# Optimization experiments

Hardware: AMD Instinct MI355X
Metric: run time of the kernel (lower is better)

## Reference

```python
import jax, jax.numpy as jnp
import numpy as np

B = 16384
QD = 2048   # query_dim
KD = 1024   # key_dim
HID = 1024  # hidden_dim = min(QD, KD)
NH = 16     # num_heads
HD = HID // NH  # head_dim = 64
LN_EPS = 1e-5


def _ln(x, w, b):
    m = jnp.mean(x, axis=-1, keepdims=True)
    v = jnp.mean((x - m) ** 2, axis=-1, keepdims=True)
    return (x - m) * jax.lax.rsqrt(v + LN_EPS) * w + b


def _lin(x, W, b):
    return x @ W.T + b


def setup_inputs() -> dict:
    key = jax.random.key(0)
    ks = jax.random.split(key, 12)
    p = lambda k, shape: jax.random.normal(k, shape, jnp.float32) * 0.02
    return dict(
        query_features=jax.random.normal(ks[0], (B, QD), jnp.float32),
        key_features=jax.random.normal(ks[1], (B, KD), jnp.float32),
        Wq=p(ks[2], (HID, QD)), bq=jnp.zeros((HID,), jnp.float32),
        ln_q_w=jnp.ones((HID,), jnp.float32), ln_q_b=jnp.zeros((HID,), jnp.float32),
        Wk=p(ks[3], (HID, KD)), bk=jnp.zeros((HID,), jnp.float32),
        ln_k_w=jnp.ones((HID,), jnp.float32), ln_k_b=jnp.zeros((HID,), jnp.float32),
        Wvq=p(ks[4], (HID, QD)), bvq=jnp.zeros((HID,), jnp.float32),
        Wvk=p(ks[5], (HID, KD)), bvk=jnp.zeros((HID,), jnp.float32),
        Wo=p(ks[6], (QD, HID)), bo=jnp.zeros((QD,), jnp.float32),
        ln_o_w=jnp.ones((QD,), jnp.float32), ln_o_b=jnp.zeros((QD,), jnp.float32),
        Wg1=p(ks[7], (HID, QD + KD)), bg1=jnp.zeros((HID,), jnp.float32),
        Wg2=p(ks[8], (1, HID)), bg2=jnp.zeros((1,), jnp.float32),
        Wc1=p(ks[9], (HID, QD + KD)), bc1=jnp.zeros((HID,), jnp.float32),
        Wc2=p(ks[10], (1, HID)), bc2=jnp.zeros((1,), jnp.float32),
    )


def reference(query_features, key_features,
              Wq, bq, ln_q_w, ln_q_b,
              Wk, bk, ln_k_w, ln_k_b,
              Wvq, bvq, Wvk, bvk,
              Wo, bo, ln_o_w, ln_o_b,
              Wg1, bg1, Wg2, bg2,
              Wc1, bc1, Wc2, bc2):
    b = query_features.shape[0]
    q = _ln(_lin(query_features, Wq, bq), ln_q_w, ln_q_b)      # [B, HID]
    k = _ln(_lin(key_features, Wk, bk), ln_k_w, ln_k_b)        # [B, HID]
    v_q = _lin(query_features, Wvq, bvq)  # computed in torch but unused
    v_k = _lin(key_features, Wvk, bvk)    # [B, HID]
    q = q.reshape(b, NH, HD)
    k = k.reshape(b, NH, HD)
    v_k = v_k.reshape(b, NH, HD)
    # NOTE: attention mixes over the HEAD axis (j == num_heads), per original einsum
    scores = jnp.einsum('bhd,bjd->bhj', q, k) / np.sqrt(HD).astype(np.float32)
    attn = jax.nn.softmax(scores, axis=-1)  # dropout p effectively 0 / eval mode
    attended = jnp.einsum('bhj,bjd->bhd', attn, v_k).reshape(b, HID)
    output = _ln(_lin(attended, Wo, bo), ln_o_w, ln_o_b)       # [B, QD]
    combined = jnp.concatenate([query_features, key_features], axis=1)  # [B, QD+KD]
    gate = jax.nn.sigmoid(_lin(jax.nn.gelu(_lin(combined, Wg1, bg1), approximate=False), Wg2, bg2))
    chem = jax.nn.sigmoid(_lin(jax.nn.gelu(_lin(combined, Wc1, bc1), approximate=False), Wc2, bc2))
    effective_gate = gate * chem  # [B, 1]
    return query_features + effective_gate * output
```

## Files before the change

kernel.cpp:

```cpp
#include <hip/hip_runtime.h>
#include <stdint.h>

#define QD 2048
#define KD 1024
#define HID 1024
#define NH 16
#define HD 64
#define CMBD 3072

typedef float  f32x4   __attribute__((ext_vector_type(4)));
typedef short  short8  __attribute__((ext_vector_type(8)));
typedef short  short4v __attribute__((ext_vector_type(4)));
typedef float  float4v __attribute__((ext_vector_type(4)));

__device__ inline float bf2f(short s) {
  unsigned u = ((unsigned)(unsigned short)s) << 16;
  return __builtin_bit_cast(float, u);
}
__device__ inline short f2bf(float f) {
  unsigned u = __builtin_bit_cast(unsigned, f);
  u = u + 0x7fff + ((u >> 16) & 1);
  return (short)(u >> 16);
}
__device__ inline unsigned char f2f8(float f) {
  unsigned u = __builtin_bit_cast(unsigned, f);
  unsigned s = (u >> 24) & 0x80u;
  float a = fabsf(f);
  if (a >= 448.f) return (unsigned char)(s | 0x7E);
  if (a < 0.015625f) {
    int m = (int)(a * 512.f + 0.5f);
    if (m > 7) return (unsigned char)(s | 0x08);
    return (unsigned char)(s | m);
  }
  int ebits = (int)((u >> 23) & 0xFF) - 127;
  unsigned mant = u & 0x7FFFFF;
  unsigned keep = mant >> 20;
  unsigned rest = mant & 0xFFFFF;
  keep += (rest > 0x80000u) || (rest == 0x80000u && (keep & 1));
  if (keep == 8) { keep = 0; ebits += 1; }
  if (ebits > 8) return (unsigned char)(s | 0x7E);
  return (unsigned char)(s | ((unsigned)(ebits + 7) << 3) | keep);
}

__global__ void cvt_inputs(const float* __restrict__ qf, const float* __restrict__ kf,
                           short* __restrict__ cmb, unsigned char* __restrict__ cmb8,
                           int rows2) {
  const int b = blockIdx.x, t = threadIdx.x;
  int row, c4, base;
  const float* src;
  if (b < rows2) { const int i = b * 256 + t; row = i >> 9; c4 = i & 511; base = 0;  src = qf + (size_t)row * QD + c4 * 4; }
  else           { const int i = (b - rows2) * 256 + t; row = i >> 8; c4 = i & 255; base = QD; src = kf + (size_t)row * KD + c4 * 4; }
  float4v v = *(const float4v*)src;
  short4v o;
  o[0] = f2bf(v[0]); o[1] = f2bf(v[1]); o[2] = f2bf(v[2]); o[3] = f2bf(v[3]);
  *(short4v*)(cmb + (size_t)row * CMBD + base + c4 * 4) = o;
  unsigned p = (unsigned)f2f8(v[0]) | ((unsigned)f2f8(v[1]) << 8) |
               ((unsigned)f2f8(v[2]) << 16) | ((unsigned)f2f8(v[3]) << 24);
  *(unsigned*)(cmb8 + (size_t)row * CMBD + base + c4 * 4) = p;
}

struct WSeg { const float* s; short* d; int blkEnd; };
__global__ void cvt_weights(WSeg s0, WSeg s1, WSeg s2, WSeg s3) {
  int b = blockIdx.x;
  WSeg seg; int base;
  if      (b < s0.blkEnd) { seg = s0; base = 0; }
  else if (b < s1.blkEnd) { seg = s1; base = s0.blkEnd; }
  else if (b < s2.blkEnd) { seg = s2; base = s1.blkEnd; }
  else                    { seg = s3; base = s2.blkEnd; }
  const size_t i = ((size_t)(b - base) * 256 + threadIdx.x) * 4;
  float4v v = *(const float4v*)(seg.s + i);
  short4v o;
  o[0] = f2bf(v[0]); o[1] = f2bf(v[1]); o[2] = f2bf(v[2]); o[3] = f2bf(v[3]);
  *(short4v*)(seg.d + i) = o;
}

__global__ void cvt_w8(const float* __restrict__ Wg1, const float* __restrict__ Wc1,
                       unsigned char* __restrict__ wgc8, int half) {
  const int b = blockIdx.x;
  const float* s = (b < half) ? Wg1 : Wc1;
  unsigned char* d = wgc8 + (b < half ? 0 : (size_t)HID * CMBD);
  const size_t i = ((size_t)(b < half ? b : b - half) * 256 + threadIdx.x) * 4;
  float4v v = *(const float4v*)(s + i);
  unsigned p = (unsigned)f2f8(v[0]) | ((unsigned)f2f8(v[1]) << 8) |
               ((unsigned)f2f8(v[2]) << 16) | ((unsigned)f2f8(v[3]) << 24);
  *(unsigned*)(d + i) = p;
}

__global__ void pack_params(float* __restrict__ egp, int egpN,
                            const float* __restrict__ bg1, const float* __restrict__ bc1,
                            const float* __restrict__ bk,  const float* __restrict__ bvk,
                            const float* __restrict__ Wg2, const float* __restrict__ Wc2,
                            float* __restrict__ bgc, float* __restrict__ bkv,
                            float* __restrict__ w2gc) {
  int i = blockIdx.x * 256 + threadIdx.x;
  if (i < egpN) { egp[i] = 0.f; return; }
  i -= egpN;
  const int seg = i >> 10, idx = i & 1023;
  switch (seg) {
    case 0: bgc[idx]         = bg1[idx]; break;
    case 1: bgc[1024 + idx]  = bc1[idx]; break;
    case 2: bkv[idx]         = bk[idx];  break;
    case 3: bkv[1024 + idx]  = bvk[idx]; break;
    case 4: w2gc[idx]        = Wg2[idx]; break;
    case 5: w2gc[1024 + idx] = Wc2[idx]; break;
  }
}

#define EPI_NONE 0
#define EPI_GATE 2

typedef const __attribute__((address_space(1))) void gvoid_t;
typedef __attribute__((address_space(3))) void lvoid_t;

#define WAIT_VM(n)  asm volatile("s_waitcnt vmcnt(" #n ")" ::: "memory")

#define APAN(b, kp) (((b) * 2 + (kp)) * 8192)
#define BPAN(b, kp) (32768 + ((b) * 2 + (kp)) * 8192)

#define PHASE_MID                                        \
  __builtin_amdgcn_s_barrier();                          \
  asm volatile("s_waitcnt lgkmcnt(0)" ::: "memory");     \
  __builtin_amdgcn_s_setprio(1);

#define PHASE_END                                        \
  __builtin_amdgcn_s_setprio(0);                         \
  __builtin_amdgcn_s_barrier();

template<int EPI>
__global__ __launch_bounds__(512, 2)
void gemm256(const short* __restrict__ A, size_t lda,
             const short* __restrict__ W,
             const float* __restrict__ bias,
             short* __restrict__ C, int N, int K,
             const float* __restrict__ w2, float* __restrict__ egp, int rowsTot) {
  extern __shared__ short ls[];
  const int tid  = threadIdx.x;
  const int lane = tid & 63;
  const int wave = tid >> 6;
  const int wm = wave >> 2, wn = wave & 3;
  const int fr = lane & 15, kq4 = lane >> 4;

  const int nwg = gridDim.x * gridDim.y;
  const int lin = blockIdx.y * gridDim.x + blockIdx.x;
  const int cpx = nwg >> 3;
  const int nid = (lin & 7) * cpx + (lin >> 3);
  const int bx = nid % gridDim.x, by = nid / gridDim.x;
  const size_t rowBase = (size_t)by * 256;
  const size_t colBase = (size_t)bx * 256;

  const int NTT = K >> 6;

  f32x4 acc[8][4];
#pragma unroll
  for (int mi = 0; mi < 8; mi++)
#pragma unroll
    for (int ni = 0; ni < 4; ni++) acc[mi][ni] = (f32x4){0.f, 0.f, 0.f, 0.f};

  const int frsw = (kq4 ^ ((fr >> 1) & 3)) * 8;

  const int grow  = tid >> 2;
  const int slotx = (tid & 3) ^ ((tid >> 3) & 3);
  const short* gAlo = A + (rowBase + grow) * lda + slotx * 8;
  const short* gAhi = gAlo + (size_t)128 * lda;
  const short* gBlo = W + (colBase + grow) * (size_t)K + slotx * 8;
  const short* gBhi = gBlo + (size_t)128 * K;
  short* const sdst = ls + tid * 8;

  auto STG_A = [&](int panOff, int kcol) {
    __builtin_amdgcn_global_load_lds((gvoid_t*)(gAlo + kcol), (lvoid_t*)(sdst + panOff),        16, 0, 0);
    __builtin_amdgcn_global_load_lds((gvoid_t*)(gAhi + kcol), (lvoid_t*)(sdst + panOff + 4096), 16, 0, 0);
  };
  auto STG_B = [&](int panOff, int kcol) {
    __builtin_amdgcn_global_load_lds((gvoid_t*)(gBlo + kcol), (lvoid_t*)(sdst + panOff),        16, 0, 0);
    __builtin_amdgcn_global_load_lds((gvoid_t*)(gBhi + kcol), (lvoid_t*)(sdst + panOff + 4096), 16, 0, 0);
  };

  STG_A(APAN(0, 0), 0);  STG_A(APAN(0, 1), 32);
  STG_B(BPAN(0, 0), 0);  STG_B(BPAN(0, 1), 32);
  STG_B(BPAN(1, 0), 64); STG_B(BPAN(1, 1), 96);
  WAIT_VM(4);
  __builtin_amdgcn_s_barrier();

  short8 fa0[8], fa1[8], fb0[4], fb1[4];

  for (int t = 0; t < NTT; t += 2) {
    const bool more = (t + 2 < NTT);
    const int kA1 = (t + 1) * 64;
    const int kE2 = (t + 2) * 64;
    const int kO3 = (t + 3) * 64;

#pragma unroll
    for (int m = 0; m < 4; m++) {
      const int r = (wm * 128 + m * 16 + fr) * 32 + frsw;
      fa0[m * 2 + 0] = *(const short8*)(ls + APAN(0, 0) + r);
      fa0[m * 2 + 1] = *(const short8*)(ls + APAN(0, 1) + r);
    }
#pragma unroll
    for (int n = 0; n < 2; n++) {
      const int r = (wn * 64 + n * 16 + fr) * 32 + frsw;
      fb0[n * 2 + 0] = *(const short8*)(ls + BPAN(0, 0) + r);
      fb0[n * 2 + 1] = *(const short8*)(ls + BPAN(0, 1) + r);
    }
    STG_A(APAN(1, 0), kA1);
    PHASE_MID
#pragma unroll
    for (int m = 0; m < 4; m++)
#pragma unroll
      for (int n = 0; n < 2; n++) {
        acc[m][n] = __builtin_amdgcn_mfma_f32_16x16x32_bf16(fa0[m*2+0], fb0[n*2+0], acc[m][n], 0, 0, 0);
        acc[m][n] = __builtin_amdgcn_mfma_f32_16x16x32_bf16(fa0[m*2+1], fb0[n*2+1], acc[m][n], 0, 0, 0);
      }
    PHASE_END

#pragma unroll
    for (int n = 0; n < 2; n++) {
      const int r = (wn * 64 + (n + 2) * 16 + fr) * 32 + frsw;
      fb1[n * 2 + 0] = *(const short8*)(ls + BPAN(0, 0) + r);
      fb1[n * 2 + 1] = *(const short8*)(ls + BPAN(0, 1) + r);
    }
    STG_A(APAN(1, 1), kA1 + 32);
    PHASE_MID
#pragma unroll
    for (int m = 0; m < 4; m++)
#pragma unroll
      for (int n = 0; n < 2; n++) {
        acc[m][n+2] = __builtin_amdgcn_mfma_f32_16x16x32_bf16(fa0[m*2+0], fb1[n*2+0], acc[m][n+2], 0, 0, 0);
        acc[m][n+2] = __builtin_amdgcn_mfma_f32_16x16x32_bf16(fa0[m*2+1], fb1[n*2+1], acc[m][n+2], 0, 0, 0);
      }
    PHASE_END

#pragma unroll
    for (int m = 0; m < 4; m++) {
      const int r = (wm * 128 + (m + 4) * 16 + fr) * 32 + frsw;
      fa1[m * 2 + 0] = *(const short8*)(ls + APAN(0, 0) + r);
      fa1[m * 2 + 1] = *(const short8*)(ls + APAN(0, 1) + r);
    }
    if (more) STG_B(BPAN(0, 0), kE2);
    PHASE_MID
#pragma unroll
    for (int m = 0; m < 4; m++)
#pragma unroll
      for (int n = 0; n < 2; n++) {
        acc[m+4][n] = __builtin_amdgcn_mfma_f32_16x16x32_bf16(fa1[m*2+0], fb0[n*2+0], acc[m+4][n], 0, 0, 0);
        acc[m+4][n] = __builtin_amdgcn_mfma_f32_16x16x32_bf16(fa1[m*2+1], fb0[n*2+1], acc[m+4][n], 0, 0, 0);
      }
    PHASE_END

    if (more) STG_B(BPAN(0, 1), kE2 + 32);
    PHASE_MID
#pragma unroll
    for (int m = 0; m < 4; m++)
#pragma unroll
      for (int n = 0; n < 2; n++) {
        acc[m+4][n+2] = __builtin_amdgcn_mfma_f32_16x16x32_bf16(fa1[m*2+0], fb1[n*2+0], acc[m+4][n+2], 0, 0, 0);
        acc[m+4][n+2] = __builtin_amdgcn_mfma_f32_16x16x32_bf16(fa1[m*2+1], fb1[n*2+1], acc[m+4][n+2], 0, 0, 0);
      }
    __builtin_amdgcn_s_setprio(0);
    if (more) { WAIT_VM(4); } else { WAIT_VM(0); }
    __builtin_amdgcn_s_barrier();

#pragma unroll
    for (int m = 0; m < 4; m++) {
      const int r = (wm * 128 + m * 16 + fr) * 32 + frsw;
      fa0[m * 2 + 0] = *(const short8*)(ls + APAN(1, 0) + r);
      fa0[m * 2 + 1] = *(const short8*)(ls + APAN(1, 1) + r);
    }
#pragma unroll
    for (int n = 0; n < 2; n++) {
      const int r = (wn * 64 + n * 16 + fr) * 32 + frsw;
      fb0[n * 2 + 0] = *(const short8*)(ls + BPAN(1, 0) + r);
      fb0[n * 2 + 1] = *(const short8*)(ls + BPAN(1, 1) + r);
    }
    if (more) STG_A(APAN(0, 0), kE2);
    PHASE_MID
#pragma unroll
    for (int m = 0; m < 4; m++)
#pragma unroll
      for (int n = 0; n < 2; n++) {
        acc[m][n] = __builtin_amdgcn_mfma_f32_16x16x32_bf16(fa0[m*2+0], fb0[n*2+0], acc[m][n], 0, 0, 0);
        acc[m][n] = __builtin_amdgcn_mfma_f32_16x16x32_bf16(fa0[m*2+1], fb0[n*2+1], acc[m][n], 0, 0, 0);
      }
    PHASE_END

#pragma unroll
    for (int n = 0; n < 2; n++) {
      const int r = (wn * 64 + (n + 2) * 16 + fr) * 32 + frsw;
      fb1[n * 2 + 0] = *(const short8*)(ls + BPAN(1, 0) + r);
      fb1[n * 2 + 1] = *(const short8*)(ls + BPAN(1, 1) + r);
    }
    if (more) STG_A(APAN(0, 1), kE2 + 32);
    PHASE_MID
#pragma unroll
    for (int m = 0; m < 4; m++)
#pragma unroll
      for (int n = 0; n < 2; n++) {
        acc[m][n+2] = __builtin_amdgcn_mfma_f32_16x16x32_bf16(fa0[m*2+0], fb1[n*2+0], acc[m][n+2], 0, 0, 0);
        acc[m][n+2] = __builtin_amdgcn_mfma_f32_16x16x32_bf16(fa0[m*2+1], fb1[n*2+1], acc[m][n+2], 0, 0, 0);
      }
    PHASE_END

#pragma unroll
    for (int m = 0; m < 4; m++) {
      const int r = (wm * 128 + (m + 4) * 16 + fr) * 32 + frsw;
      fa1[m * 2 + 0] = *(const short8*)(ls + APAN(1, 0) + r);
      fa1[m * 2 + 1] = *(const short8*)(ls + APAN(1, 1) + r);
    }
    if (more) STG_B(BPAN(1, 0), kO3);
    PHASE_MID
#pragma unroll
    for (int m = 0; m < 4; m++)
#pragma unroll
      for (int n = 0; n < 2; n++) {
        acc[m+4][n] = __builtin_amdgcn_mfma_f32_16x16x32_bf16(fa1[m*2+0], fb0[n*2+0], acc[m+4][n], 0, 0, 0);
        acc[m+4][n] = __builtin_amdgcn_mfma_f32_16x16x32_bf16(fa1[m*2+1], fb0[n*2+1], acc[m+4][n], 0, 0, 0);
      }
    PHASE_END

    if (more) STG_B(BPAN(1, 1), kO3 + 32);
    PHASE_MID
#pragma unroll
    for (int m = 0; m < 4; m++)
#pragma unroll
      for (int n = 0; n < 2; n++) {
        acc[m+4][n+2] = __builtin_amdgcn_mfma_f32_16x16x32_bf16(fa1[m*2+0], fb1[n*2+0], acc[m+4][n+2], 0, 0, 0);
        acc[m+4][n+2] = __builtin_amdgcn_mfma_f32_16x16x32_bf16(fa1[m*2+1], fb1[n*2+1], acc[m+4][n+2], 0, 0, 0);
      }
    __builtin_amdgcn_s_setprio(0);
    if (more) { WAIT_VM(4); }
    __builtin_amdgcn_s_barrier();
  }

#pragma unroll
  for (int mi = 0; mi < 8; mi++) {
    const size_t row0 = rowBase + wm * 128 + mi * 16 + kq4 * 4;
#pragma unroll
    for (int ni = 0; ni < 4; ni++) {
      const int col = (int)colBase + wn * 64 + ni * 16 + fr;
      const float bv = bias[col];
#pragma unroll
      for (int j = 0; j < 4; j++) {
        float x = acc[mi][ni][j] + bv;
        C[(row0 + j) * (size_t)N + col] = f2bf(x);
      }
    }
  }
}

__global__ __launch_bounds__(512, 2)
void gemm_gate8(const unsigned char* __restrict__ A,
                const unsigned char* __restrict__ W,
                const float* __restrict__ bias,
                const float* __restrict__ w2, float* __restrict__ egp, int rowsTot) {
  __shared__ unsigned char ls[65536];
  const int tid  = threadIdx.x;
  const int lane = tid & 63;
  const int wave = tid >> 6;
  const int wm = wave >> 2, wn = wave & 3;
  const int fr = lane & 15, kq4 = lane >> 4;

  const int nwg = gridDim.x * gridDim.y;
  const int lin = blockIdx.y * gridDim.x + blockIdx.x;
  const int cpx = nwg >> 3;
  const int nid = (lin & 7) * cpx + (lin >> 3);
  const int bx = nid % gridDim.x, by = nid / gridDim.x;
  const size_t rowBase = (size_t)by * 256;
  const size_t colBase = (size_t)bx * 256;

  const int NTT = CMBD >> 6;

  f32x4 acc[8][4];
#pragma unroll
  for (int mi = 0; mi < 8; mi++)
#pragma unroll
    for (int ni = 0; ni < 4; ni++) acc[mi][ni] = (f32x4){0.f, 0.f, 0.f, 0.f};

  const int g16 = (((kq4 >> 1) ^ ((fr >> 2) & 1)) << 4) + (kq4 & 1) * 8;
  const int aoff = (wm * 128 + fr) * 32 + g16;
  const int boff = 32768 + (wn * 64 + fr) * 32 + g16;

  const int srow = tid >> 1;
  const int sg   = (tid & 1) ^ ((tid >> 3) & 1);
  const unsigned char* gA = A + (rowBase + srow) * (size_t)CMBD + sg * 16;
  const unsigned char* gB = W + (colBase + srow) * (size_t)CMBD + sg * 16;
  unsigned char* const sdst = ls + tid * 16;

  auto STG_A = [&](int panOff, int kcol) {
    __builtin_amdgcn_global_load_lds((gvoid_t*)(gA + kcol), (lvoid_t*)(sdst + panOff), 16, 0, 0);
  };
  auto STG_B = [&](int panOff, int kcol) {
    __builtin_amdgcn_global_load_lds((gvoid_t*)(gB + kcol), (lvoid_t*)(sdst + panOff + 32768), 16, 0, 0);
  };

  STG_A(APAN(0, 0), 0);  STG_A(APAN(0, 1), 32);
  STG_B(APAN(0, 0), 0);  STG_B(APAN(0, 1), 32);
  STG_B(APAN(1, 0), 64); STG_B(APAN(1, 1), 96);
  WAIT_VM(2);
  __builtin_amdgcn_s_barrier();

  long long fa0[8], fa1[8], fb0[4], fb1[4];

  for (int t = 0; t < NTT; t += 2) {
    const bool more = (t + 2 < NTT);
    const int kA1 = (t + 1) * 64;
    const int kE2 = (t + 2) * 64;
    const int kO3 = (t + 3) * 64;

#pragma unroll
    for (int m = 0; m < 4; m++) {
      const int r = aoff + m * 512;
      fa0[m * 2 + 0] = *(const long long*)(ls + APAN(0, 0) + r);
      fa0[m * 2 + 1] = *(const long long*)(ls + APAN(0, 1) + r);
    }
#pragma unroll
    for (int n = 0; n < 2; n++) {
      const int r = boff + n * 512;
      fb0[n * 2 + 0] = *(const long long*)(ls + APAN(0, 0) + r);
      fb0[n * 2 + 1] = *(const long long*)(ls + APAN(0, 1) + r);
    }
    STG_A(APAN(1, 0), kA1);
    PHASE_MID
#pragma unroll
    for (int m = 0; m < 4; m++)
#pragma unroll
      for (int n = 0; n < 2; n++) {
        acc[m][n] = __builtin_amdgcn_mfma_f32_16x16x32_fp8_fp8(fa0[m*2+0], fb0[n*2+0], acc[m][n], 0, 0, 0);
        acc[m][n] = __builtin_amdgcn_mfma_f32_16x16x32_fp8_fp8(fa0[m*2+1], fb0[n*2+1], acc[m][n], 0, 0, 0);
      }
    PHASE_END

#pragma unroll
    for (int n = 0; n < 2; n++) {
      const int r = boff + (n + 2) * 512;
      fb1[n * 2 + 0] = *(const long long*)(ls + APAN(0, 0) + r);
      fb1[n * 2 + 1] = *(const long long*)(ls + APAN(0, 1) + r);
    }
    STG_A(APAN(1, 1), kA1 + 32);
    PHASE_MID
#pragma unroll
    for (int m = 0; m < 4; m++)
#pragma unroll
      for (int n = 0; n < 2; n++) {
        acc[m][n+2] = __builtin_amdgcn_mfma_f32_16x16x32_fp8_fp8(fa0[m*2+0], fb1[n*2+0], acc[m][n+2], 0, 0, 0);
        acc[m][n+2] = __builtin_amdgcn_mfma_f32_16x16x32_fp8_fp8(fa0[m*2+1], fb1[n*2+1], acc[m][n+2], 0, 0, 0);
      }
    PHASE_END

#pragma unroll
    for (int m = 0; m < 4; m++) {
      const int r = aoff + (m + 4) * 512;
      fa1[m * 2 + 0] = *(const long long*)(ls + APAN(0, 0) + r);
      fa1[m * 2 + 1] = *(const long long*)(ls + APAN(0, 1) + r);
    }
    if (more) STG_B(APAN(0, 0), kE2);
    PHASE_MID
#pragma unroll
    for (int m = 0; m < 4; m++)
#pragma unroll
      for (int n = 0; n < 2; n++) {
        acc[m+4][n] = __builtin_amdgcn_mfma_f32_16x16x32_fp8_fp8(fa1[m*2+0], fb0[n*2+0], acc[m+4][n], 0, 0, 0);
        acc[m+4][n] = __builtin_amdgcn_mfma_f32_16x16x32_fp8_fp8(fa1[m*2+1], fb0[n*2+1], acc[m+4][n], 0, 0, 0);
      }
    PHASE_END

    if (more) STG_B(APAN(0, 1), kE2 + 32);
    PHASE_MID
#pragma unroll
    for (int m = 0; m < 4; m++)
#pragma unroll
      for (int n = 0; n < 2; n++) {
        acc[m+4][n+2] = __builtin_amdgcn_mfma_f32_16x16x32_fp8_fp8(fa1[m*2+0], fb1[n*2+0], acc[m+4][n+2], 0, 0, 0);
        acc[m+4][n+2] = __builtin_amdgcn_mfma_f32_16x16x32_fp8_fp8(fa1[m*2+1], fb1[n*2+1], acc[m+4][n+2], 0, 0, 0);
      }
    __builtin_amdgcn_s_setprio(0);
    if (more) { WAIT_VM(2); } else { WAIT_VM(0); }
    __builtin_amdgcn_s_barrier();

#pragma unroll
    for (int m = 0; m < 4; m++) {
      const int r = aoff + m * 512;
      fa0[m * 2 + 0] = *(const long long*)(ls + APAN(1, 0) + r);
      fa0[m * 2 + 1] = *(const long long*)(ls + APAN(1, 1) + r);
    }
#pragma unroll
    for (int n = 0; n < 2; n++) {
      const int r = boff + n * 512;
      fb0[n * 2 + 0] = *(const long long*)(ls + APAN(1, 0) + r);
      fb0[n * 2 + 1] = *(const long long*)(ls + APAN(1, 1) + r);
    }
    if (more) STG_A(APAN(0, 0), kE2);
    PHASE_MID
#pragma unroll
    for (int m = 0; m < 4; m++)
#pragma unroll
      for (int n = 0; n < 2; n++) {
        acc[m][n] = __builtin_amdgcn_mfma_f32_16x16x32_fp8_fp8(fa0[m*2+0], fb0[n*2+0], acc[m][n], 0, 0, 0);
        acc[m][n] = __builtin_amdgcn_mfma_f32_16x16x32_fp8_fp8(fa0[m*2+1], fb0[n*2+1], acc[m][n], 0, 0, 0);
      }
    PHASE_END

#pragma unroll
    for (int n = 0; n < 2; n++) {
      const int r = boff + (n + 2) * 512;
      fb1[n * 2 + 0] = *(const long long*)(ls + APAN(1, 0) + r);
      fb1[n * 2 + 1] = *(const long long*)(ls + APAN(1, 1) + r);
    }
    if (more) STG_A(APAN(0, 1), kE2 + 32);
    PHASE_MID
#pragma unroll
    for (int m = 0; m < 4; m++)
#pragma unroll
      for (int n = 0; n < 2; n++) {
        acc[m][n+2] = __builtin_amdgcn_mfma_f32_16x16x32_fp8_fp8(fa0[m*2+0], fb1[n*2+0], acc[m][n+2], 0, 0, 0);
        acc[m][n+2] = __builtin_amdgcn_mfma_f32_16x16x32_fp8_fp8(fa0[m*2+1], fb1[n*2+1], acc[m][n+2], 0, 0, 0);
      }
    PHASE_END

#pragma unroll
    for (int m = 0; m < 4; m++) {
      const int r = aoff + (m + 4) * 512;
      fa1[m * 2 + 0] = *(const long long*)(ls + APAN(1, 0) + r);
      fa1[m * 2 + 1] = *(const long long*)(ls + APAN(1, 1) + r);
    }
    if (more) STG_B(APAN(1, 0), kO3);
    PHASE_MID
#pragma unroll
    for (int m = 0; m < 4; m++)
#pragma unroll
      for (int n = 0; n < 2; n++) {
        acc[m+4][n] = __builtin_amdgcn_mfma_f32_16x16x32_fp8_fp8(fa1[m*2+0], fb0[n*2+0], acc[m+4][n], 0, 0, 0);
        acc[m+4][n] = __builtin_amdgcn_mfma_f32_16x16x32_fp8_fp8(fa1[m*2+1], fb0[n*2+1], acc[m+4][n], 0, 0, 0);
      }
    PHASE_END

    if (more) STG_B(APAN(1, 1), kO3 + 32);
    PHASE_MID
#pragma unroll
    for (int m = 0; m < 4; m++)
#pragma unroll
      for (int n = 0; n < 2; n++) {
        acc[m+4][n+2] = __builtin_amdgcn_mfma_f32_16x16x32_fp8_fp8(fa1[m*2+0], fb1[n*2+0], acc[m+4][n+2], 0, 0, 0);
        acc[m+4][n+2] = __builtin_amdgcn_mfma_f32_16x16x32_fp8_fp8(fa1[m*2+1], fb1[n*2+1], acc[m+4][n+2], 0, 0, 0);
      }
    __builtin_amdgcn_s_setprio(0);
    if (more) { WAIT_VM(2); }
    __builtin_amdgcn_s_barrier();
  }

  float w2v[4], bvv[4];
#pragma unroll
  for (int ni = 0; ni < 4; ni++) {
    const int c = (int)colBase + wn * 64 + ni * 16 + fr;
    w2v[ni] = w2[c]; bvv[ni] = bias[c];
  }
  const int half = (colBase >= 1024) ? 1 : 0;
#pragma unroll
  for (int mi = 0; mi < 8; mi++) {
    float sj[4] = {0.f, 0.f, 0.f, 0.f};
#pragma unroll
    for (int ni = 0; ni < 4; ni++)
#pragma unroll
      for (int j = 0; j < 4; j++) {
        float x = acc[mi][ni][j] + bvv[ni];
        float g = 0.5f * x * (1.f + erff(x * 0.70710678118f));
        sj[j] += g * w2v[ni];
      }
#pragma unroll
    for (int j = 0; j < 4; j++) {
#pragma unroll
      for (int o = 8; o >= 1; o >>= 1) sj[j] += __shfl_xor(sj[j], o);
      if (fr == 0) {
        const int row = (int)rowBase + wm * 128 + mi * 16 + kq4 * 4 + j;
        atomicAdd(egp + half * rowsTot + row, sj[j]);
      }
    }
  }
}

__device__ inline float4 block_sum4(float a, float b, float c, float d, float* sc) {
#pragma unroll
  for (int o = 32; o >= 1; o >>= 1) {
    a += __shfl_down(a, o); b += __shfl_down(b, o);
    c += __shfl_down(c, o); d += __shfl_down(d, o);
  }
  const int lane = threadIdx.x & 63, w = threadIdx.x >> 6;
  const int nw = blockDim.x >> 6;
  if (lane == 0) { sc[w*4] = a; sc[w*4+1] = b; sc[w*4+2] = c; sc[w*4+3] = d; }
  __syncthreads();
  float ra = 0.f, rb = 0.f, rc = 0.f, rd = 0.f;
  for (int i = 0; i < nw; i++) { ra += sc[i*4]; rb += sc[i*4+1]; rc += sc[i*4+2]; rd += sc[i*4+3]; }
  __syncthreads();
  return make_float4(ra, rb, rc, rd);
}
__device__ inline float2 block_sum2(float a, float b, float* sc) {
#pragma unroll
  for (int o = 32; o >= 1; o >>= 1) { a += __shfl_down(a, o); b += __shfl_down(b, o); }
  const int lane = threadIdx.x & 63, w = threadIdx.x >> 6;
  const int nw = blockDim.x >> 6;
  if (lane == 0) { sc[w*2] = a; sc[w*2+1] = b; }
  __syncthreads();
  float ra = 0.f, rb = 0.f;
  for (int i = 0; i < nw; i++) { ra += sc[i*2]; rb += sc[i*2+1]; }
  __syncthreads();
  return make_float2(ra, rb);
}

__global__ __launch_bounds__(256)
void attn_ln(const short* __restrict__ qp, const short* __restrict__ kv,
             const float* __restrict__ lnqw, const float* __restrict__ lnqb,
             const float* __restrict__ lnkw, const float* __restrict__ lnkb,
             short* __restrict__ att) {
  __shared__ float qs[HID];
  __shared__ float ks[NH * 65];
  __shared__ float vs[HID];
  __shared__ float aw[256];
  __shared__ float red[16];
  const int t = threadIdx.x;
  const size_t row = blockIdx.x;

  short4v q4 = *(const short4v*)(qp + row * HID + t * 4);
  short4v k4 = *(const short4v*)(kv + row * 2048 + t * 4);
  short4v v4 = *(const short4v*)(kv + row * 2048 + 1024 + t * 4);
  float qv[4], kvv[4];
  float sq = 0.f, sqq = 0.f, sk = 0.f, skk = 0.f;
#pragma unroll
  for (int i = 0; i < 4; i++) {
    qv[i] = bf2f(q4[i]); sq += qv[i]; sqq += qv[i] * qv[i];
    kvv[i] = bf2f(k4[i]); sk += kvv[i]; skk += kvv[i] * kvv[i];
  }
  float4 r4 = block_sum4(sq, sqq, sk, skk, red);
  float mq = r4.x / HID, vq = r4.y / HID - mq * mq;
  float rsq = rsqrtf(vq + 1e-5f);
  float mk = r4.z / HID, vv = r4.w / HID - mk * mk;
  float rsk = rsqrtf(vv + 1e-5f);
#pragma unroll
  for (int i = 0; i < 4; i++) {
    const int idx = t * 4 + i;
    qs[idx] = (qv[i] - mq) * rsq * lnqw[idx] + lnqb[idx];
    ks[(idx >> 6) * 65 + (idx & 63)] = (kvv[i] - mk) * rsk * lnkw[idx] + lnkb[idx];
    vs[idx] = bf2f(v4[i]);
  }
  __syncthreads();

  const int h = t >> 4, j = t & 15;
  float s = 0.f;
#pragma unroll 8
  for (int d = 0; d < 64; d++) s += qs[h * 64 + d] * ks[j * 65 + d];
  s *= 0.125f;
  float mx = s;
#pragma unroll
  for (int o = 8; o >= 1; o >>= 1) mx = fmaxf(mx, __shfl_xor(mx, o, 16));
  float e = __expf(s - mx);
  float sum = e;
#pragma unroll
  for (int o = 8; o >= 1; o >>= 1) sum += __shfl_xor(sum, o, 16);
  aw[t] = e / sum;
  __syncthreads();

  const int dB = (t & 15) * 4;
  float o0 = 0.f, o1 = 0.f, o2 = 0.f, o3 = 0.f;
#pragma unroll
  for (int jj = 0; jj < 16; jj++) {
    const float w = aw[h * 16 + jj];
    const float* vp = &vs[jj * 64 + dB];
    o0 += w * vp[0]; o1 += w * vp[1]; o2 += w * vp[2]; o3 += w * vp[3];
  }
  short4v o4;
  o4[0] = f2bf(o0); o4[1] = f2bf(o1); o4[2] = f2bf(o2); o4[3] = f2bf(o3);
  *(short4v*)(att + row * HID + h * 64 + dB) = o4;
}

__global__ __launch_bounds__(256)
void final_kernel(const short* __restrict__ opre, const short* __restrict__ cmb,
                  const float* __restrict__ egp, int rowsTot,
                  const float* __restrict__ bg2, const float* __restrict__ bc2,
                  const float* __restrict__ lnow, const float* __restrict__ lnob,
                  float* __restrict__ out) {
  __shared__ float red[8];
  const int t = threadIdx.x;
  const size_t row = blockIdx.x;
  short8 o8 = *(const short8*)(opre + row * QD + t * 8);
  short8 q8 = *(const short8*)(cmb + row * CMBD + t * 8);
  float x[8];
  float s = 0.f, ss = 0.f;
#pragma unroll
  for (int i = 0; i < 8; i++) { x[i] = bf2f(o8[i]); s += x[i]; ss += x[i] * x[i]; }
  float2 r = block_sum2(s, ss, red);
  float m = r.x / QD, v = r.y / QD - m * m;
  float rs = rsqrtf(v + 1e-5f);
  float gg = 1.f / (1.f + __expf(-(egp[row] + bg2[0])));
  float gc = 1.f / (1.f + __expf(-(egp[rowsTot + row] + bc2[0])));
  float g = gg * gc;
  float4v oa, ob;
#pragma unroll
  for (int i = 0; i < 8; i++) {
    const int c = t * 8 + i;
    float y = (x[i] - m) * rs * lnow[c] + lnob[c];
    float r2 = bf2f(q8[i]) + g * y;
    if (i < 4) oa[i] = r2; else ob[i - 4] = r2;
  }
  *(float4v*)(out + row * QD + t * 8) = oa;
  *(float4v*)(out + row * QD + t * 8 + 4) = ob;
}

extern "C" void kernel_launch(void* const* d_in, const int* in_sizes, int n_in,
                              void* d_out, int out_size, void* d_ws, size_t ws_size,
                              hipStream_t stream) {
  const float* qf   = (const float*)d_in[0];
  const float* kf   = (const float*)d_in[1];
  const float* Wq   = (const float*)d_in[2];
  const float* bq   = (const float*)d_in[3];
  const float* lnqw = (const float*)d_in[4];
  const float* lnqb = (const float*)d_in[5];
  const float* Wk   = (const float*)d_in[6];
  const float* bk   = (const float*)d_in[7];
  const float* lnkw = (const float*)d_in[8];
  const float* lnkb = (const float*)d_in[9];
  const float* Wvk  = (const float*)d_in[12];
  const float* bvk  = (const float*)d_in[13];
  const float* Wo   = (const float*)d_in[14];
  const float* bo   = (const float*)d_in[15];
  const float* lnow = (const float*)d_in[16];
  const float* lnob = (const float*)d_in[17];
  const float* Wg1  = (const float*)d_in[18];
  const float* bg1  = (const float*)d_in[19];
  const float* Wg2  = (const float*)d_in[20];
  const float* bg2  = (const float*)d_in[21];
  const float* Wc1  = (const float*)d_in[22];
  const float* bc1  = (const float*)d_in[23];
  const float* Wc2  = (const float*)d_in[24];
  const float* bc2  = (const float*)d_in[25];

  const int rows = in_sizes[0] / QD;

  char* ws = (char*)d_ws;
  size_t off = 0;
  auto alloc = [&](size_t bytes) -> char* {
    char* p = ws + off;
    off += (bytes + 255) & ~(size_t)255;
    return p;
  };
  short* cmb  = (short*)alloc((size_t)rows * CMBD * 2);
  short* wqb  = (short*)alloc((size_t)HID * QD * 2);
  short* wkv  = (short*)alloc((size_t)2 * HID * KD * 2);
  short* wob  = (short*)alloc((size_t)QD * HID * 2);
  unsigned char* wgc8 = (unsigned char*)alloc((size_t)2 * HID * CMBD);
  short* hgc  = (short*)alloc((size_t)rows * 2048 * 2);
  short* qp   = (short*)alloc((size_t)rows * HID * 2);
  short* kvp  = (short*)alloc((size_t)rows * 2048 * 2);
  float* egp  = (float*)alloc((size_t)2 * rows * 4);
  float* bgc  = (float*)alloc(2048 * 4);
  float* bkv  = (float*)alloc(2048 * 4);
  float* w2gc = (float*)alloc(2048 * 4);
  short* att  = hgc;
  unsigned char* cmb8 = (unsigned char*)hgc;
  short* opre = kvp;

  const int egpN = 2 * rows;
  pack_params<<<(egpN + 6144) / 256, 256, 0, stream>>>(egp, egpN, bg1, bc1, bk, bvk,
                                                       Wg2, Wc2, bgc, bkv, w2gc);

  cvt_inputs<<<rows * 3, 256, 0, stream>>>(qf, kf, cmb, cmb8, rows * 2);
  {
    WSeg s0{Wq,  wqb,                    2048};
    WSeg s1{Wk,  wkv,                    2048 + 1024};
    WSeg s2{Wvk, wkv + (size_t)HID * KD, 2048 + 2048};
    WSeg s3{Wo,  wob,                    2048 + 2048 + 2048};
    cvt_weights<<<s3.blkEnd, 256, 0, stream>>>(s0, s1, s2, s3);
  }
  cvt_w8<<<6144, 256, 0, stream>>>(Wg1, Wc1, wgc8, 3072);

  hipFuncSetAttribute((const void*)gemm256<EPI_NONE>,
                      hipFuncAttributeMaxDynamicSharedMemorySize, 131072);

  const dim3 blk(512);
  const int mt = rows / 256;
  const size_t lds = 131072;

  gemm_gate8<<<dim3(8, mt), blk, 0, stream>>>(cmb8, wgc8, bgc, w2gc, egp, rows);
  gemm256<EPI_NONE><<<dim3(1024 / 256, mt), blk, lds, stream>>>(cmb, CMBD, wqb, bq, qp, 1024, QD, nullptr, nullptr, 0);
  gemm256<EPI_NONE><<<dim3(2048 / 256, mt), blk, lds, stream>>>(cmb + QD, CMBD, wkv, bkv, kvp, 2048, KD, nullptr, nullptr, 0);
  attn_ln<<<rows, 256, 0, stream>>>(qp, kvp, lnqw, lnqb, lnkw, lnkb, att);
  gemm256<EPI_NONE><<<dim3(2048 / 256, mt), blk, lds, stream>>>(att, HID, wob, bo, opre, 2048, HID, nullptr, nullptr, 0);
  final_kernel<<<rows, 256, 0, stream>>>(opre, cmb, egp, rows, bg2, bc2, lnow, lnob, (float*)d_out);
}
```

Baseline: 591.3 us.

## Pre-tile FP8 operands into LDS-ready panel layout for contiguous gate GEMM loads

The FP8 conversion kernels now write activations and gate weights in a blocked layout matching the LDS fragment order (256-row bands, 32-wide k tiles, 16x8 groups). The FP8 gate GEMM can then stage each k-tile with one contiguous 8 KB global_load_lds per panel, with no swizzling and simpler LDS fragment addressing. Input conversion also processes 8 elements per thread. The costs are scattered 8-byte stores in the conversion kernels and a layout the gate GEMM and converters must agree on exactly.

Result: slower. 632.8 us (+7.0%).

```diff
diff --git a/kernel.cpp b/kernel.cpp
--- a/kernel.cpp
+++ b/kernel.cpp
@@ -42,21 +42,32 @@
   return (unsigned char)(s | ((unsigned)(ebits + 7) << 3) | keep);
 }
 
+__device__ inline size_t fp8addr(int r, int k) {
+  return (size_t)(r >> 8) * 786432 + (size_t)(k >> 5) * 8192 +
+         (size_t)((r >> 4) & 15) * 512 + (size_t)((k >> 3) & 3) * 128 +
+         (size_t)(r & 15) * 8;
+}
+
 __global__ void cvt_inputs(const float* __restrict__ qf, const float* __restrict__ kf,
                            short* __restrict__ cmb, unsigned char* __restrict__ cmb8,
-                           int rows2) {
+                           int qblocks) {
   const int b = blockIdx.x, t = threadIdx.x;
-  int row, c4, base;
+  int r, k;
   const float* src;
-  if (b < rows2) { const int i = b * 256 + t; row = i >> 9; c4 = i & 511; base = 0;  src = qf + (size_t)row * QD + c4 * 4; }
-  else           { const int i = (b - rows2) * 256 + t; row = i >> 8; c4 = i & 255; base = QD; src = kf + (size_t)row * KD + c4 * 4; }
-  float4v v = *(const float4v*)src;
-  short4v o;
-  o[0] = f2bf(v[0]); o[1] = f2bf(v[1]); o[2] = f2bf(v[2]); o[3] = f2bf(v[3]);
-  *(short4v*)(cmb + (size_t)row * CMBD + base + c4 * 4) = o;
-  unsigned p = (unsigned)f2f8(v[0]) | ((unsigned)f2f8(v[1]) << 8) |
-               ((unsigned)f2f8(v[2]) << 16) | ((unsigned)f2f8(v[3]) << 24);
-  *(unsigned*)(cmb8 + (size_t)row * CMBD + base + c4 * 4) = p;
+  if (b < qblocks) { const int i = b * 256 + t; r = i >> 8; k = (i & 255) * 8; src = qf + (size_t)r * QD + k; }
+  else             { const int i = (b - qblocks) * 256 + t; r = i >> 7; k = (i & 127) * 8; src = kf + (size_t)r * KD + k; k += QD; }
+  float4v v0 = *(const float4v*)src;
+  float4v v1 = *(const float4v*)(src + 4);
+  short8 o;
+  o[0] = f2bf(v0[0]); o[1] = f2bf(v0[1]); o[2] = f2bf(v0[2]); o[3] = f2bf(v0[3]);
+  o[4] = f2bf(v1[0]); o[5] = f2bf(v1[1]); o[6] = f2bf(v1[2]); o[7] = f2bf(v1[3]);
+  *(short8*)(cmb + (size_t)r * CMBD + k) = o;
+  unsigned long long p =
+      (unsigned long long)f2f8(v0[0])        | ((unsigned long long)f2f8(v0[1]) << 8)  |
+      ((unsigned long long)f2f8(v0[2]) << 16)| ((unsigned long long)f2f8(v0[3]) << 24) |
+      ((unsigned long long)f2f8(v1[0]) << 32)| ((unsigned long long)f2f8(v1[1]) << 40) |
+      ((unsigned long long)f2f8(v1[2]) << 48)| ((unsigned long long)f2f8(v1[3]) << 56);
+  *(unsigned long long*)(cmb8 + fp8addr(r, k)) = p;
 }
 
 struct WSeg { const float* s; short* d; int blkEnd; };
@@ -75,15 +86,23 @@
 }
 
 __global__ void cvt_w8(const float* __restrict__ Wg1, const float* __restrict__ Wc1,
-                       unsigned char* __restrict__ wgc8, int half) {
-  const int b = blockIdx.x;
-  const float* s = (b < half) ? Wg1 : Wc1;
-  unsigned char* d = wgc8 + (b < half ? 0 : (size_t)HID * CMBD);
-  const size_t i = ((size_t)(b < half ? b : b - half) * 256 + threadIdx.x) * 4;
-  float4v v = *(const float4v*)(s + i);
-  unsigned p = (unsigned)f2f8(v[0]) | ((unsigned)f2f8(v[1]) << 8) |
-               ((unsigned)f2f8(v[2]) << 16) | ((unsigned)f2f8(v[3]) << 24);
-  *(unsigned*)(d + i) = p;
+                       unsigned char* __restrict__ wgc8) {
+  const int kt = blockIdx.x, band = blockIdx.y;
+  unsigned char* dst = wgc8 + (size_t)band * 786432 + (size_t)kt * 8192;
+  for (int p = threadIdx.x; p < 1024; p += 256) {
+    const int grp = p >> 6, kq = (p >> 4) & 3, fr = p & 15;
+    const int c = band * 256 + grp * 16 + fr;
+    const int k = kt * 32 + kq * 8;
+    const float* s = (c < 1024 ? Wg1 + (size_t)c * CMBD : Wc1 + (size_t)(c - 1024) * CMBD) + k;
+    float4v v0 = *(const float4v*)s;
+    float4v v1 = *(const float4v*)(s + 4);
+    unsigned long long pk =
+        (unsigned long long)f2f8(v0[0])        | ((unsigned long long)f2f8(v0[1]) << 8)  |
+        ((unsigned long long)f2f8(v0[2]) << 16)| ((unsigned long long)f2f8(v0[3]) << 24) |
+        ((unsigned long long)f2f8(v1[0]) << 32)| ((unsigned long long)f2f8(v1[1]) << 40) |
+        ((unsigned long long)f2f8(v1[2]) << 48)| ((unsigned long long)f2f8(v1[3]) << 56);
+    *(unsigned long long*)(dst + p * 8) = pk;
+  }
 }
 
 __global__ void pack_params(float* __restrict__ egp, int egpN,
@@ -107,7 +126,6 @@
 }
 
 #define EPI_NONE 0
-#define EPI_GATE 2
 
 typedef const __attribute__((address_space(1))) void gvoid_t;
 typedef __attribute__((address_space(3))) void lvoid_t;
@@ -374,26 +392,22 @@
 #pragma unroll
     for (int ni = 0; ni < 4; ni++) acc[mi][ni] = (f32x4){0.f, 0.f, 0.f, 0.f};
 
-  const int g16 = (((kq4 >> 1) ^ ((fr >> 2) & 1)) << 4) + (kq4 & 1) * 8;
-  const int aoff = (wm * 128 + fr) * 32 + g16;
-  const int boff = 32768 + (wn * 64 + fr) * 32 + g16;
-
-  const int srow = tid >> 1;
-  const int sg   = (tid & 1) ^ ((tid >> 3) & 1);
-  const unsigned char* gA = A + (rowBase + srow) * (size_t)CMBD + sg * 16;
-  const unsigned char* gB = W + (colBase + srow) * (size_t)CMBD + sg * 16;
+  const int lp = kq4 * 128 + fr * 8;
+
+  const unsigned char* gA = A + (size_t)by * 786432 + tid * 16;
+  const unsigned char* gB = W + (size_t)bx * 786432 + tid * 16;
   unsigned char* const sdst = ls + tid * 16;
 
-  auto STG_A = [&](int panOff, int kcol) {
-    __builtin_amdgcn_global_load_lds((gvoid_t*)(gA + kcol), (lvoid_t*)(sdst + panOff), 16, 0, 0);
+  auto STG_A = [&](int panOff, int kt) {
+    __builtin_amdgcn_global_load_lds((gvoid_t*)(gA + (size_t)kt * 8192), (lvoid_t*)(sdst + panOff), 16, 0, 0);
   };
-  auto STG_B = [&](int panOff, int kcol) {
-    __builtin_amdgcn_global_load_lds((gvoid_t*)(gB + kcol), (lvoid_t*)(sdst + panOff + 32768), 16, 0, 0);
+  auto STG_B = [&](int panOff, int kt) {
+    __builtin_amdgcn_global_load_lds((gvoid_t*)(gB + (size_t)kt * 8192), (lvoid_t*)(sdst + 32768 + panOff), 16, 0, 0);
   };
 
-  STG_A(APAN(0, 0), 0);  STG_A(APAN(0, 1), 32);
-  STG_B(APAN(0, 0), 0);  STG_B(APAN(0, 1), 32);
-  STG_B(APAN(1, 0), 64); STG_B(APAN(1, 1), 96);
+  STG_A(APAN(0, 0), 0); STG_A(APAN(0, 1), 1);
+  STG_B(APAN(0, 0), 0); STG_B(APAN(0, 1), 1);
+  STG_B(APAN(1, 0), 2); STG_B(APAN(1, 1), 3);
   WAIT_VM(2);
   __builtin_amdgcn_s_barrier();
 
@@ -401,23 +415,21 @@
 
   for (int t = 0; t < NTT; t += 2) {
     const bool more = (t + 2 < NTT);
-    const int kA1 = (t + 1) * 64;
-    const int kE2 = (t + 2) * 64;
-    const int kO3 = (t + 3) * 64;
+    const int k1 = 2 * (t + 1), k2 = 2 * (t + 2), k3 = 2 * (t + 3);
 
 #pragma unroll
     for (int m = 0; m < 4; m++) {
-      const int r = aoff + m * 512;
+      const int r = (wm * 8 + m) * 512 + lp;
       fa0[m * 2 + 0] = *(const long long*)(ls + APAN(0, 0) + r);
       fa0[m * 2 + 1] = *(const long long*)(ls + APAN(0, 1) + r);
     }
 #pragma unroll
     for (int n = 0; n < 2; n++) {
-      const int r = boff + n * 512;
+      const int r = 32768 + (wn * 4 + n) * 512 + lp;
       fb0[n * 2 + 0] = *(const long long*)(ls + APAN(0, 0) + r);
       fb0[n * 2 + 1] = *(const long long*)(ls + APAN(0, 1) + r);
     }
-    STG_A(APAN(1, 0), kA1);
+    STG_A(APAN(1, 0), k1);
     PHASE_MID
 #pragma unroll
     for (int m = 0; m < 4; m++)
@@ -430,11 +442,11 @@
 
 #pragma unroll
     for (int n = 0; n < 2; n++) {
-      const int r = boff + (n + 2) * 512;
+      const int r = 32768 + (wn * 4 + n + 2) * 512 + lp;
       fb1[n * 2 + 0] = *(const long long*)(ls + APAN(0, 0) + r);
       fb1[n * 2 + 1] = *(const long long*)(ls + APAN(0, 1) + r);
     }
-    STG_A(APAN(1, 1), kA1 + 32);
+    STG_A(APAN(1, 1), k1 + 1);
     PHASE_MID
 #pragma unroll
     for (int m = 0; m < 4; m++)
@@ -447,11 +459,11 @@
 
 #pragma unroll
     for (int m = 0; m < 4; m++) {
-      const int r = aoff + (m + 4) * 512;
+      const int r = (wm * 8 + m + 4) * 512 + lp;
       fa1[m * 2 + 0] = *(const long long*)(ls + APAN(0, 0) + r);
       fa1[m * 2 + 1] = *(const long long*)(ls + APAN(0, 1) + r);
     }
-    if (more) STG_B(APAN(0, 0), kE2);
+    if (more) STG_B(APAN(0, 0), k2);
     PHASE_MID
 #pragma unroll
     for (int m = 0; m < 4; m++)
@@ -462,7 +474,7 @@
       }
     PHASE_END
 
-    if (more) STG_B(APAN(0, 1), kE2 + 32);
+    if (more) STG_B(APAN(0, 1), k2 + 1);
     PHASE_MID
 #pragma unroll
     for (int m = 0; m < 4; m++)
@@ -477,17 +489,17 @@
 
 #pragma unroll
     for (int m = 0; m < 4; m++) {
-      const int r = aoff + m * 512;
+      const int r = (wm * 8 + m) * 512 + lp;
       fa0[m * 2 + 0] = *(const long long*)(ls + APAN(1, 0) + r);
       fa0[m * 2 + 1] = *(const long long*)(ls + APAN(1, 1) + r);
     }
 #pragma unroll
     for (int n = 0; n < 2; n++) {
-      const int r = boff + n * 512;
+      const int r = 32768 + (wn * 4 + n) * 512 + lp;
       fb0[n * 2 + 0] = *(const long long*)(ls + APAN(1, 0) + r);
       fb0[n * 2 + 1] = *(const long long*)(ls + APAN(1, 1) + r);
     }
-    if (more) STG_A(APAN(0, 0), kE2);
+    if (more) STG_A(APAN(0, 0), k2);
     PHASE_MID
 #pragma unroll
     for (int m = 0; m < 4; m++)
@@ -500,11 +512,11 @@
 
 #pragma unroll
     for (int n = 0; n < 2; n++) {
-      const int r = boff + (n + 2) * 512;
+      const int r = 32768 + (wn * 4 + n + 2) * 512 + lp;
       fb1[n * 2 + 0] = *(const long long*)(ls + APAN(1, 0) + r);
       fb1[n * 2 + 1] = *(const long long*)(ls + APAN(1, 1) + r);
     }
-    if (more) STG_A(APAN(0, 1), kE2 + 32);
+    if (more) STG_A(APAN(0, 1), k2 + 1);
     PHASE_MID
 #pragma unroll
     for (int m = 0; m < 4; m++)
@@ -517,11 +529,11 @@
 
 #pragma unroll
     for (int m = 0; m < 4; m++) {
-      const int r = aoff + (m + 4) * 512;
+      const int r = (wm * 8 + m + 4) * 512 + lp;
       fa1[m * 2 + 0] = *(const long long*)(ls + APAN(1, 0) + r);
       fa1[m * 2 + 1] = *(const long long*)(ls + APAN(1, 1) + r);
     }
-    if (more) STG_B(APAN(1, 0), kO3);
+    if (more) STG_B(APAN(1, 0), k3);
     PHASE_MID
 #pragma unroll
     for (int m = 0; m < 4; m++)
@@ -532,7 +544,7 @@
       }
     PHASE_END
 
-    if (more) STG_B(APAN(1, 1), kO3 + 32);
+    if (more) STG_B(APAN(1, 1), k3 + 1);
     PHASE_MID
 #pragma unroll
     for (int m = 0; m < 4; m++)
@@ -759,7 +771,9 @@
   pack_params<<<(egpN + 6144) / 256, 256, 0, stream>>>(egp, egpN, bg1, bc1, bk, bvk,
                                                        Wg2, Wc2, bgc, bkv, w2gc);
 
-  cvt_inputs<<<rows * 3, 256, 0, stream>>>(qf, kf, cmb, cmb8, rows * 2);
+  const int qblocks = rows * QD / 8 / 256;
+  const int kblocks = rows * KD / 8 / 256;
+  cvt_inputs<<<qblocks + kblocks, 256, 0, stream>>>(qf, kf, cmb, cmb8, qblocks);
   {
     WSeg s0{Wq,  wqb,                    2048};
     WSeg s1{Wk,  wkv,                    2048 + 1024};
@@ -767,7 +781,7 @@
     WSeg s3{Wo,  wob,                    2048 + 2048 + 2048};
     cvt_weights<<<s3.blkEnd, 256, 0, stream>>>(s0, s1, s2, s3);
   }
-  cvt_w8<<<6144, 256, 0, stream>>>(Wg1, Wc1, wgc8, 3072);
+  cvt_w8<<<dim3(96, 8), 256, 0, stream>>>(Wg1, Wc1, wgc8);
 
   hipFuncSetAttribute((const void*)gemm256<EPI_NONE>,
                       hipFuncAttributeMaxDynamicSharedMemorySize, 131072);
```
